# Kernel optimization log

Measured on AMD Instinct MI355X. Metric: run time of the kernel, lower is better.

The kernel has to match this reference:

```python
import jax, jax.numpy as jnp
import numpy as np

D_MODEL = 2048
N_HEADS = 16
N_KV_HEADS = 4
HEAD_DIM = D_MODEL // N_HEADS  # 128
ROPE_BASE = 10000.0


def _rope_tables(T, head_dim):
    half = head_dim // 2
    theta = 1.0 / (ROPE_BASE ** (jnp.arange(half, dtype=jnp.float32) / half))
    m = jnp.arange(T, dtype=jnp.float32)
    freqs = jnp.outer(m, theta)  # (T, half)
    return jnp.cos(freqs), jnp.sin(freqs)


def _apply_rope(x, cos, sin):
    # x: (B, H, T, hd); rotate first/second halves as pairs
    half = x.shape[-1] // 2
    x1, x2 = x[..., :half], x[..., half:]
    cos = cos[None, None, :, :]
    sin = sin[None, None, :, :]
    return jnp.concatenate([x1 * cos - x2 * sin, x1 * sin + x2 * cos], axis=-1)


def setup_inputs() -> dict:
    key = jax.random.key(0)
    ks = jax.random.split(key, 5)
    B, T = 4, 2048
    x = jax.random.normal(ks[0], (B, T, D_MODEL), dtype=jnp.float32)
    Wq = jax.random.normal(ks[1], (D_MODEL, N_HEADS * HEAD_DIM), dtype=jnp.float32) * 0.02
    Wk = jax.random.normal(ks[2], (D_MODEL, N_KV_HEADS * HEAD_DIM), dtype=jnp.float32) * 0.02
    Wv = jax.random.normal(ks[3], (D_MODEL, N_KV_HEADS * HEAD_DIM), dtype=jnp.float32) * 0.02
    Wo = jax.random.normal(ks[4], (N_HEADS * HEAD_DIM, D_MODEL), dtype=jnp.float32) * (0.02 / np.sqrt(2.0))
    return {"x": x, "Wq": Wq, "Wk": Wk, "Wv": Wv, "Wo": Wo}


def reference(x, Wq, Wk, Wv, Wo):
    B, T, C = x.shape
    groups = N_HEADS // N_KV_HEADS

    # QKV projections
    q = (x @ Wq).reshape(B, T, N_HEADS, HEAD_DIM).transpose(0, 2, 1, 3)      # (B,H,T,hd)
    k = (x @ Wk).reshape(B, T, N_KV_HEADS, HEAD_DIM).transpose(0, 2, 1, 3)   # (B,Hkv,T,hd)
    v = (x @ Wv).reshape(B, T, N_KV_HEADS, HEAD_DIM).transpose(0, 2, 1, 3)

    # RoPE on q and k
    cos, sin = _rope_tables(T, HEAD_DIM)
    q = _apply_rope(q, cos, sin)
    k = _apply_rope(k, cos, sin)

    # GQA: repeat each kv head `groups` times
    k = jnp.repeat(k, groups, axis=1)  # (B,H,T,hd)
    v = jnp.repeat(v, groups, axis=1)

    # Attention scores with ALiBi bias and causal mask
    scale = 1.0 / np.sqrt(HEAD_DIM)
    scores = jnp.einsum('bhqd,bhkd->bhqk', q, k) * scale  # (B,H,T,T)

    pos = jnp.arange(T)
    dist = jnp.minimum(pos[None, :] - pos[:, None], 0).astype(jnp.float32)  # (T,T), <=0
    slopes = 2.0 ** (-8.0 * jnp.arange(1, N_HEADS + 1, dtype=jnp.float32) / N_HEADS)
    alibi = slopes[:, None, None] * dist[None, :, :]  # (H,T,T)
    scores = scores + alibi[None]

    causal = pos[None, :] > pos[:, None]  # True = future = blocked
    scores = jnp.where(causal[None, None], -jnp.inf, scores)

    weights = jax.nn.softmax(scores, axis=-1)
    out = jnp.einsum('bhqk,bhkd->bhqd', weights, v)  # (B,H,T,hd)
    out = out.transpose(0, 2, 1, 3).reshape(B, T, N_HEADS * HEAD_DIM)
    return out @ Wo
```

## Files before the change

### kernel.cpp

```cpp
#include <hip/hip_runtime.h>
#include <hip/hip_bf16.h>
#include <stdint.h>

#define T_SEQ 2048
#define DM    2048
#define NH    16
#define NKVH  4
#define HD    128
#define NBATCH 4
#define BT    (NBATCH * T_SEQ)
#define ATT_SCALE 0.08838834764831845f
#define LOG2E 1.4426950408889634f

typedef __attribute__((ext_vector_type(8))) short bf16x8;
typedef __attribute__((ext_vector_type(4))) float f32x4;
typedef __attribute__((ext_vector_type(16))) float f32x16;
typedef __attribute__((ext_vector_type(8))) unsigned short ushort8;
typedef __attribute__((ext_vector_type(4))) unsigned short ushort4v;

static __device__ __forceinline__ unsigned short f2bf(float f) {
  __hip_bfloat16 h = __float2bfloat16(f);
  return __builtin_bit_cast(unsigned short, h);
}
static __device__ __forceinline__ float bf2f(unsigned short u) {
  unsigned int v = ((unsigned int)u) << 16;
  return __builtin_bit_cast(float, v);
}
static __device__ __forceinline__ unsigned int cvtpk(float a, float b) {
  unsigned int r;
  asm("v_cvt_pk_bf16_f32 %0, %1, %2" : "=v"(r) : "v"(a), "v"(b));
  return r;
}

#define GLDS16(g, l)                                                        \
  __builtin_amdgcn_global_load_lds(                                         \
      (const __attribute__((address_space(1))) void*)(g),                   \
      (__attribute__((address_space(3))) void*)(l), 16, 0, 0)

__global__ __launch_bounds__(256) void castx_k(const float* __restrict__ x,
                                               unsigned short* __restrict__ xb) {
  int i = (blockIdx.x * 256 + threadIdx.x) * 4;
  float4 v = *(const float4*)&x[i];
  ushort4v o;
  o[0] = f2bf(v.x); o[1] = f2bf(v.y); o[2] = f2bf(v.z); o[3] = f2bf(v.w);
  *(ushort4v*)&xb[i] = o;
}

__global__ __launch_bounds__(256) void transqkv_k(const float* __restrict__ Wq,
                                                  const float* __restrict__ Wk,
                                                  const float* __restrict__ Wv,
                                                  unsigned short* __restrict__ wqt) {
  __shared__ unsigned short t[64][72];
  const int bx = blockIdx.x;
  const float* src;
  unsigned short* dst;
  int ncols, n0;
  if (bx < 32) {
    src = Wq; dst = wqt; ncols = 2048; n0 = bx * 64;
  } else if (bx < 40) {
    src = Wk; dst = wqt + (size_t)2048 * 2048; ncols = 512; n0 = (bx - 32) * 64;
  } else {
    src = Wv; dst = wqt + (size_t)2560 * 2048; ncols = 512; n0 = (bx - 40) * 64;
  }
  const int r0 = blockIdx.y * 64;
  const int tid = threadIdx.x;
  const int tx = tid & 15, ty = tid >> 4;
#pragma unroll
  for (int i = 0; i < 4; i++) {
    int r = ty * 4 + i;
    float4 v = *(const float4*)&src[(size_t)(r0 + r) * ncols + n0 + tx * 4];
    t[r][tx * 4 + 0] = f2bf(v.x);
    t[r][tx * 4 + 1] = f2bf(v.y);
    t[r][tx * 4 + 2] = f2bf(v.z);
    t[r][tx * 4 + 3] = f2bf(v.w);
  }
  __syncthreads();
  int nl = tid >> 2, seg = tid & 3;
  ushort8 o0, o1;
#pragma unroll
  for (int j = 0; j < 8; j++) {
    o0[j] = t[seg * 16 + j][nl];
    o1[j] = t[seg * 16 + 8 + j][nl];
  }
  size_t base = (size_t)(n0 + nl) * 2048 + r0 + seg * 16;
  *(ushort8*)&dst[base] = o0;
  *(ushort8*)&dst[base + 8] = o1;
}

__global__ __launch_bounds__(256) void transw_k(const float* __restrict__ src,
                                                unsigned short* __restrict__ dst,
                                                int ncols) {
  __shared__ unsigned short t[64][72];
  int n0 = blockIdx.x * 64, r0 = blockIdx.y * 64;
  int tid = threadIdx.x;
  int tx = tid & 15, ty = tid >> 4;
#pragma unroll
  for (int i = 0; i < 4; i++) {
    int r = ty * 4 + i;
    float4 v = *(const float4*)&src[(size_t)(r0 + r) * ncols + n0 + tx * 4];
    t[r][tx * 4 + 0] = f2bf(v.x);
    t[r][tx * 4 + 1] = f2bf(v.y);
    t[r][tx * 4 + 2] = f2bf(v.z);
    t[r][tx * 4 + 3] = f2bf(v.w);
  }
  __syncthreads();
  int nl = tid >> 2, seg = tid & 3;
  ushort8 o0, o1;
#pragma unroll
  for (int j = 0; j < 8; j++) {
    o0[j] = t[seg * 16 + j][nl];
    o1[j] = t[seg * 16 + 8 + j][nl];
  }
  size_t base = (size_t)(n0 + nl) * 2048 + r0 + seg * 16;
  *(ushort8*)&dst[base] = o0;
  *(ushort8*)&dst[base + 8] = o1;
}

template <int EPI, int NBY, int BYG>
__global__ __launch_bounds__(512) void gemm8_k(const unsigned short* __restrict__ A,
                                               const unsigned short* __restrict__ Bt,
                                               unsigned short* __restrict__ q_out,
                                               unsigned short* __restrict__ k_out,
                                               unsigned short* __restrict__ v_out,
                                               float* __restrict__ f_out) {
  __shared__ __align__(16) unsigned short smem[65536];

  const int tid = threadIdx.x;
  const int lane = tid & 63, wid = tid >> 6;
  const int wm = wid >> 2, wn = wid & 3;
  const int lr = lane & 15, lq = lane >> 4;
  const int sw = ((lr >> 2) & 1) << 1;

  const int k8 = blockIdx.x & 7;
  const int l = blockIdx.x >> 3;
  const int gi = l / (4 * BYG);
  const int t4 = l % (4 * BYG);
  const int bx = k8 * 4 + (t4 & 3);
  const int by = gi * BYG + (t4 >> 2);
  const int row0 = bx * 256, n00 = by * 256;

  const int clog = (tid & 7) ^ (((tid >> 5) & 1) << 1);
  const unsigned short* Asrc = A + (size_t)row0 * 2048 + clog * 8;
  const unsigned short* Bsrc = Bt + (size_t)n00 * 2048 + clog * 8;

  auto stageA = [&](int buf, int h, int k0) {
#pragma unroll
    for (int c = 0; c < 2; c++) {
      const int rl = c * 128 + h * 64 + (tid >> 3);
      GLDS16(Asrc + (size_t)rl * 2048 + k0,
             &smem[buf * 32768 + (c * 128 + h * 64) * 64 + tid * 8]);
    }
  };
  auto stageB = [&](int buf, int h, int k0) {
#pragma unroll
    for (int c = 0; c < 2; c++) {
      const int pr = h * 128 + c * 64 + (tid >> 3);
      const int p = pr >> 5;
      const int lg = (p < 4) ? (2 * p) : (2 * (p - 4) + 1);
      const int logical = lg * 32 + (pr & 31);
      GLDS16(Bsrc + (size_t)logical * 2048 + k0,
             &smem[buf * 32768 + 16384 + (h * 128 + c * 64) * 64 + tid * 8]);
    }
  };

  auto ldA = [&](int buf, int rl, int kh) -> bf16x8 {
    return *(const bf16x8*)&smem[buf * 32768 + rl * 64 + (((kh << 2) + lq) ^ sw) * 8];
  };
  auto ldB = [&](int buf, int ni, int kh) -> bf16x8 {
    const int p = (ni < 2) ? wn : (4 + wn);
    const int pr = p * 32 + (ni & 1) * 16 + lr;
    return *(const bf16x8*)&smem[buf * 32768 + 16384 + pr * 64 +
                                 (((kh << 2) + lq) ^ sw) * 8];
  };

  f32x4 acc[8][4] = {};

  stageA(0, 0, 0);
  stageB(0, 0, 0);
  stageB(0, 1, 0);
  stageA(0, 1, 0);

  bf16x8 af[4][2], bfr[4][2];

#pragma unroll 1
  for (int t = 0; t < 32; ++t) {
    const int buf = t & 1, obuf = buf ^ 1;
    const bool nx = (t + 1 < 32);
    const int k0n = (t + 1) << 6;

    asm volatile("s_waitcnt vmcnt(4)" ::: "memory");
    asm volatile("s_barrier" ::: "memory");
#pragma unroll
    for (int m = 0; m < 4; m++)
#pragma unroll
      for (int kh = 0; kh < 2; kh++) af[m][kh] = ldA(buf, wm * 128 + m * 16 + lr, kh);
#pragma unroll
    for (int ni = 0; ni < 2; ni++)
#pragma unroll
      for (int kh = 0; kh < 2; kh++) bfr[ni][kh] = ldB(buf, ni, kh);
    if (nx) stageA(obuf, 0, k0n);
    __builtin_amdgcn_s_setprio(1);
#pragma unroll
    for (int m = 0; m < 4; m++)
#pragma unroll
      for (int ni = 0; ni < 2; ni++)
#pragma unroll
        for (int kh = 0; kh < 2; kh++)
          acc[m][ni] = __builtin_amdgcn_mfma_f32_16x16x32_bf16(af[m][kh], bfr[ni][kh],
                                                               acc[m][ni], 0, 0, 0);
    __builtin_amdgcn_s_setprio(0);

    if (nx) asm volatile("s_waitcnt vmcnt(4)" ::: "memory");
    else    asm volatile("s_waitcnt vmcnt(2)" ::: "memory");
    asm volatile("s_barrier" ::: "memory");
#pragma unroll
    for (int ni = 2; ni < 4; ni++)
#pragma unroll
      for (int kh = 0; kh < 2; kh++) bfr[ni][kh] = ldB(buf, ni, kh);
    if (nx) stageB(obuf, 0, k0n);
    __builtin_amdgcn_s_setprio(1);
#pragma unroll
    for (int m = 0; m < 4; m++)
#pragma unroll
      for (int ni = 2; ni < 4; ni++)
#pragma unroll
        for (int kh = 0; kh < 2; kh++)
          acc[m][ni] = __builtin_amdgcn_mfma_f32_16x16x32_bf16(af[m][kh], bfr[ni][kh],
                                                               acc[m][ni], 0, 0, 0);
    __builtin_amdgcn_s_setprio(0);

    if (nx) asm volatile("s_waitcnt vmcnt(4)" ::: "memory");
    else    asm volatile("s_waitcnt vmcnt(0)" ::: "memory");
    asm volatile("s_barrier" ::: "memory");
#pragma unroll
    for (int m = 0; m < 4; m++)
#pragma unroll
      for (int kh = 0; kh < 2; kh++)
        af[m][kh] = ldA(buf, wm * 128 + 64 + m * 16 + lr, kh);
    if (nx) stageB(obuf, 1, k0n);
    __builtin_amdgcn_s_setprio(1);
#pragma unroll
    for (int m = 0; m < 4; m++)
#pragma unroll
      for (int ni = 0; ni < 2; ni++)
#pragma unroll
        for (int kh = 0; kh < 2; kh++)
          acc[4 + m][ni] = __builtin_amdgcn_mfma_f32_16x16x32_bf16(
              af[m][kh], bfr[ni][kh], acc[4 + m][ni], 0, 0, 0);
    __builtin_amdgcn_s_setprio(0);

    asm volatile("s_barrier" ::: "memory");
    if (nx) stageA(obuf, 1, k0n);
    __builtin_amdgcn_s_setprio(1);
#pragma unroll
    for (int m = 0; m < 4; m++)
#pragma unroll
      for (int ni = 2; ni < 4; ni++)
#pragma unroll
        for (int kh = 0; kh < 2; kh++)
          acc[4 + m][ni] = __builtin_amdgcn_mfma_f32_16x16x32_bf16(
              af[m][kh], bfr[ni][kh], acc[4 + m][ni], 0, 0, 0);
    __builtin_amdgcn_s_setprio(0);
  }

  const int rbase = row0 + wm * 128;
  const int cbase = n00 + wn * 64;
#pragma unroll
  for (int mi = 0; mi < 8; mi++)
#pragma unroll
    for (int ni = 0; ni < 4; ni++)
#pragma unroll
      for (int r = 0; r < 4; r++) {
        int row = rbase + mi * 16 + lq * 4 + r;
        int col = cbase + ni * 16 + lr;
        float v = acc[mi][ni][r];
        if (EPI == 0) {
          if (col < 2048) {
            q_out[(size_t)row * 2048 + col] = f2bf(v);
          } else if (col < 2560) {
            k_out[(size_t)row * 512 + (col - 2048)] = f2bf(v);
          } else {
            int nv = col - 2560;
            int kvh = nv >> 7, d = nv & 127;
            int b = row >> 11, tt = row & 2047;
            v_out[((size_t)(b * NKVH + kvh) * HD + d) * T_SEQ + tt] = f2bf(v);
          }
        } else {
          f_out[(size_t)row * 2048 + col] = v;
        }
      }
}

__global__ __launch_bounds__(256) void rope_tab_k(float2* __restrict__ tab) {
  int idx = blockIdx.x * 256 + threadIdx.x;
  int t = idx >> 6, i = idx & 63;
  float theta = exp2f(-(float)i * (13.287712379549449f / 64.0f));
  float s, c;
  sincosf((float)t * theta, &s, &c);
  tab[idx] = make_float2(c, s);
}

__global__ __launch_bounds__(256) void ropek_k(unsigned short* __restrict__ kb,
                                               const float2* __restrict__ tab) {
  int idx = blockIdx.x * 256 + threadIdx.x;
  int i = idx & 63;
  int wi = idx >> 6;
  int kvh = wi & 3;
  int bt = wi >> 2;
  int t = bt & (T_SEQ - 1);
  unsigned short* p = kb + (size_t)bt * 512 + kvh * HD;
  float2 cs = tab[(t << 6) + i];
  float x1 = bf2f(p[i]), x2 = bf2f(p[i + 64]);
  p[i] = f2bf(x1 * cs.x - x2 * cs.y);
  p[i + 64] = f2bf(x1 * cs.y + x2 * cs.x);
}

__global__ __launch_bounds__(256) void attn_k(const unsigned short* __restrict__ qb,
                                              const unsigned short* __restrict__ kb,
                                              const unsigned short* __restrict__ vt,
                                              const float2* __restrict__ rtab,
                                              unsigned short* __restrict__ ao) {
  __shared__ __align__(16) unsigned short smem[24576];

  const int bid = blockIdx.x;
  const int j = 15 - (bid >> 6);
  const int g = (bid & 7) | (((bid >> 3) & 1) << 3);
  const int hh = (bid >> 4) & 3;
  const int b = g >> 2, kvh = g & 3;
  const int h = kvh * 4 + hh;

  const int tid = threadIdx.x;
  const int wid = tid >> 6, lane = tid & 63;
  const int l31 = lane & 31, lh = lane >> 5;
  const int xr = l31 & 7;
  const float slope2 = exp2f(-0.5f * (float)(h + 1)) * LOG2E;
  const float scale2 = ATT_SCALE * LOG2E;

  const int q0 = j * 128 + wid * 32;
  const int dt_w = j * 4 + wid;
  const int nt = j * 4 + 4;

  const int krow = tid >> 4;
  const int cgk = (tid & 15) ^ (krow & 7);
  const int vr = tid >> 3;
  const int cgv = (tid & 7) ^ (vr & 7);

  const unsigned short* khead = kb + (size_t)(b * T_SEQ) * 512 + kvh * 128;
  const unsigned short* vhead = vt + (size_t)(b * NKVH + kvh) * HD * T_SEQ;

  auto stage = [&](int slot, int tile) {
    const int k0 = tile * 32;
    unsigned short* base = &smem[slot * 8192];
    GLDS16(khead + (size_t)(k0 + krow) * 512 + cgk * 8, base + tid * 8);
    GLDS16(khead + (size_t)(k0 + 16 + krow) * 512 + cgk * 8, base + 2048 + tid * 8);
    GLDS16(vhead + (size_t)(((cgv >> 2) << 6) + vr) * T_SEQ + k0 + (cgv & 3) * 8,
           base + 4096 + tid * 8);
    GLDS16(vhead + (size_t)(((cgv >> 2) << 6) + 32 + vr) * T_SEQ + k0 + (cgv & 3) * 8,
           base + 6144 + tid * 8);
  };

  unsigned short (*ot)[32][136] = (unsigned short(*)[32][136])smem;

  stage(0, nt - 1);
  stage(1, nt - 2);

  const unsigned short* qrow =
      qb + ((size_t)(b * T_SEQ + q0 + l31)) * 2048 + h * HD + lh * 8;
  bf16x8 qf[8];
#pragma unroll
  for (int ds = 0; ds < 8; ds++) qf[ds] = *(const bf16x8*)&qrow[ds * 16];

  {
    const float2* rt = rtab + ((q0 + l31) << 6) + lh * 8;
#pragma unroll
    for (int ds = 0; ds < 4; ds++)
#pragma unroll
      for (int e = 0; e < 8; e++) {
        float2 cs = rt[ds * 16 + e];
        float x1 = bf2f((unsigned short)qf[ds][e]);
        float x2 = bf2f((unsigned short)qf[ds + 4][e]);
        qf[ds][e] = (short)f2bf(x1 * cs.x - x2 * cs.y);
        qf[ds + 4][e] = (short)f2bf(x1 * cs.y + x2 * cs.x);
      }
  }

  f32x16 oacc[4] = {};
  float m2 = -1e30f, l_half = 0.f;
  const float arow = -slope2 * (float)(q0 + l31);

  float cr[16];
#pragma unroll
  for (int r = 0; r < 16; r++) {
    const int crow = (r & 3) + 8 * (r >> 2) + 4 * lh;
    cr[r] = fmaf(slope2, (float)crow, arow);
  }

#pragma unroll 1
  for (int it = 0; it < nt; ++it) {
    const int tt = nt - 1 - it;
    if (it == nt - 1) {
      asm volatile("s_waitcnt vmcnt(0)" ::: "memory");
    } else {
      asm volatile("s_waitcnt vmcnt(4)" ::: "memory");
    }
    asm volatile("s_barrier" ::: "memory");
    if (tt >= 2) stage((it + 2) % 3, tt - 2);

    if (tt <= dt_w) {
      const int slot = it % 3;
      const unsigned short* Kb = &smem[slot * 8192];
      const unsigned short* Vb = &smem[slot * 8192 + 4096];
      const int k0 = tt * 32;

      bf16x8 kf[8];
#pragma unroll
      for (int ds = 0; ds < 8; ds++)
        kf[ds] = *(const bf16x8*)&Kb[l31 * 128 + ((2 * ds + lh) ^ xr) * 8];

      __builtin_amdgcn_s_setprio(1);
      f32x16 sca = 0.f, scb = 0.f;
#pragma unroll
      for (int ds = 0; ds < 4; ds++)
        sca = __builtin_amdgcn_mfma_f32_32x32x16_bf16(kf[ds], qf[ds], sca, 0, 0, 0);
#pragma unroll
      for (int ds = 4; ds < 8; ds++)
        scb = __builtin_amdgcn_mfma_f32_32x32x16_bf16(kf[ds], qf[ds], scb, 0, 0, 0);
      __builtin_amdgcn_s_setprio(0);

      bf16x8 vf[4][2];
#pragma unroll
      for (int dt = 0; dt < 4; dt++)
#pragma unroll
        for (int ks = 0; ks < 2; ks++)
          vf[dt][ks] = *(const bf16x8*)&Vb[((dt & 1) * 32 + l31) * 64 +
                                           (((dt >> 1) * 4 + 2 * ks + lh) ^ xr) * 8];

      float s1[16];
#pragma unroll
      for (int r = 0; r < 16; r++) s1[r] = fmaf(sca[r] + scb[r], scale2, cr[r]);
      if (tt == dt_w) {
#pragma unroll
        for (int r = 0; r < 16; r++) {
          const int crow = (r & 3) + 8 * (r >> 2) + 4 * lh;
          if (crow > l31) s1[r] = -1e30f;
        }
      }

      float z = fmaf(slope2, (float)k0, -m2);

      float t8[8], t4[4];
#pragma unroll
      for (int i = 0; i < 8; i++) t8[i] = fmaxf(s1[i], s1[i + 8]);
#pragma unroll
      for (int i = 0; i < 4; i++) t4[i] = fmaxf(t8[i], t8[i + 4]);
      float mx = fmaxf(fmaxf(t4[0], t4[1]), fmaxf(t4[2], t4[3]));

      float pr[16];
#pragma unroll
      for (int r = 0; r < 16; r++) pr[r] = exp2f(s1[r] + z);

      mx = fmaxf(mx, __shfl_xor(mx, 32));
      if (__any(mx + z > 8.f)) {
        const float mt = (mx + z) + m2;
        const float mnew = fmaxf(m2, mt);
        const float corr = exp2f(m2 - mnew);
        l_half *= corr;
#pragma unroll
        for (int dt = 0; dt < 4; dt++) oacc[dt] *= corr;
        m2 = mnew;
        z = fmaf(slope2, (float)k0, -m2);
#pragma unroll
        for (int r = 0; r < 16; r++) pr[r] = exp2f(s1[r] + z);
      }

      float a8[8], a4[4];
#pragma unroll
      for (int i = 0; i < 8; i++) a8[i] = pr[i] + pr[i + 8];
#pragma unroll
      for (int i = 0; i < 4; i++) a4[i] = a8[i] + a8[i + 4];
      l_half += (a4[0] + a4[1]) + (a4[2] + a4[3]);

      unsigned int w[8];
#pragma unroll
      for (int i = 0; i < 8; i++) w[i] = cvtpk(pr[2 * i], pr[2 * i + 1]);
      const unsigned int ta = __shfl_xor(lh ? w[0] : w[2], 32);
      const unsigned int tb = __shfl_xor(lh ? w[1] : w[3], 32);
      const unsigned int tc = __shfl_xor(lh ? w[4] : w[6], 32);
      const unsigned int td = __shfl_xor(lh ? w[5] : w[7], 32);
      union U4 { unsigned int u[4]; bf16x8 v; } f0, f1;
      f0.u[0] = lh ? ta : w[0];
      f0.u[1] = lh ? tb : w[1];
      f0.u[2] = lh ? w[2] : ta;
      f0.u[3] = lh ? w[3] : tb;
      f1.u[0] = lh ? tc : w[4];
      f1.u[1] = lh ? td : w[5];
      f1.u[2] = lh ? w[6] : tc;
      f1.u[3] = lh ? w[7] : td;

      __builtin_amdgcn_s_setprio(1);
#pragma unroll
      for (int dt = 0; dt < 4; dt++) {
        oacc[dt] =
            __builtin_amdgcn_mfma_f32_32x32x16_bf16(vf[dt][0], f0.v, oacc[dt], 0, 0, 0);
        oacc[dt] =
            __builtin_amdgcn_mfma_f32_32x32x16_bf16(vf[dt][1], f1.v, oacc[dt], 0, 0, 0);
      }
      __builtin_amdgcn_s_setprio(0);
    }
  }

  const float l_tot = l_half + __shfl_xor(l_half, 32);
  const float inv = 1.0f / l_tot;
  __syncthreads();
#pragma unroll
  for (int dt = 0; dt < 4; dt++)
#pragma unroll
    for (int rg = 0; rg < 4; rg++) {
      ushort4v o;
#pragma unroll
      for (int jj = 0; jj < 4; jj++) o[jj] = f2bf(oacc[dt][rg * 4 + jj] * inv);
      *(ushort4v*)&ot[wid][l31][dt * 32 + rg * 8 + lh * 4] = o;
    }
  __syncthreads();
  const int rrow = lane >> 4, chunk = lane & 15;
#pragma unroll
  for (int ps = 0; ps < 8; ps++) {
    const int row = ps * 4 + rrow;
    ushort8 v = *(const ushort8*)&ot[wid][row][chunk * 8];
    *(ushort8*)&ao[((size_t)(b * T_SEQ + q0 + row)) * 2048 + h * HD + chunk * 8] = v;
  }
}

extern "C" void kernel_launch(void* const* d_in, const int* in_sizes, int n_in,
                              void* d_out, int out_size, void* d_ws, size_t ws_size,
                              hipStream_t stream) {
  const float* x = (const float*)d_in[0];
  const float* Wq = (const float*)d_in[1];
  const float* Wk = (const float*)d_in[2];
  const float* Wv = (const float*)d_in[3];
  const float* Wo = (const float*)d_in[4];

  char* w = (char*)d_ws;
  unsigned short* xb = (unsigned short*)w;
  unsigned short* wqt = (unsigned short*)(w + 33554432);
  unsigned short* qb = (unsigned short*)(w + 33554432 + 12582912);
  unsigned short* kb = (unsigned short*)(w + 33554432 + 12582912 + 33554432);
  unsigned short* vtb = (unsigned short*)(w + 33554432 + 12582912 + 33554432 + 8388608);
  float2* rtab = (float2*)(w + 33554432 + 8388608);

  castx_k<<<16384, 256, 0, stream>>>(x, xb);
  transqkv_k<<<dim3(48, 32), 256, 0, stream>>>(Wq, Wk, Wv, wqt);
  gemm8_k<0, 12, 3><<<384, 512, 0, stream>>>(xb, wqt, qb, kb, vtb, nullptr);
  rope_tab_k<<<512, 256, 0, stream>>>(rtab);
  ropek_k<<<8192, 256, 0, stream>>>(kb, rtab);
  transw_k<<<dim3(32, 32), 256, 0, stream>>>(Wo, wqt, 2048);
  attn_k<<<1024, 256, 0, stream>>>(qb, kb, vtb, rtab, xb);
  gemm8_k<1, 8, 4><<<256, 512, 0, stream>>>(xb, wqt, nullptr, nullptr, nullptr,
                                            (float*)d_out);
}
```

Baseline: 442.2 us.

## Replace QKV projection GEMM with 256x128-tile kernel using split B staging

Adds a new QKV projection GEMM kernel that uses 256x128 output tiles with 8 waves arranged 4x2, double-buffered LDS, and B staging split into two halves interleaved with MFMA phases. It launches 768 blocks instead of the previous 384-block wide-tile kernel. The aim is better occupancy or load balance across CUs and overlap of global loads with compute. The trade-off is less reuse per tile (more A reloads) and a scattered per-element epilogue store for the V transpose.

```diff
diff --git a/kernel.cpp b/kernel.cpp
--- a/kernel.cpp
+++ b/kernel.cpp
@@ -114,6 +114,138 @@
   size_t base = (size_t)(n0 + nl) * 2048 + r0 + seg * 16;
   *(ushort8*)&dst[base] = o0;
   *(ushort8*)&dst[base + 8] = o1;
+}
+
+__global__ __launch_bounds__(512) void gemm0n_k(const unsigned short* __restrict__ A,
+                                                const unsigned short* __restrict__ Bt,
+                                                unsigned short* __restrict__ q_out,
+                                                unsigned short* __restrict__ k_out,
+                                                unsigned short* __restrict__ v_out) {
+  __shared__ __align__(16) unsigned short smem[49152];
+
+  const int tid = threadIdx.x;
+  const int lane = tid & 63, wid = tid >> 6;
+  const int wm = wid >> 1, wn = wid & 1;
+  const int lr = lane & 15, lq = lane >> 4;
+  const int sw = ((lr >> 2) & 1) << 1;
+
+  const int k8 = blockIdx.x & 7;
+  const int l = blockIdx.x >> 3;
+  const int bx = k8 * 4 + (l & 3);
+  const int by = l >> 2;
+  const int row0 = bx * 256, n00 = by * 128;
+
+  const int clog = (tid & 7) ^ (((tid >> 5) & 1) << 1);
+  const unsigned short* Asrc = A + (size_t)row0 * 2048 + clog * 8;
+  const unsigned short* Bsrc = Bt + (size_t)n00 * 2048 + clog * 8;
+
+  auto stageA = [&](int buf, int k0) {
+#pragma unroll
+    for (int c = 0; c < 4; c++)
+      GLDS16(Asrc + (size_t)(c * 64 + (tid >> 3)) * 2048 + k0,
+             &smem[buf * 24576 + c * 4096 + tid * 8]);
+  };
+  auto stageB = [&](int buf, int h, int k0) {
+    const int pg = h * 2 + (tid >> 8);
+    const int lg = ((pg & 1) << 1) | (pg >> 1);
+    const int lrow = lg * 32 + ((tid >> 3) & 31);
+    GLDS16(Bsrc + (size_t)lrow * 2048 + k0,
+           &smem[buf * 24576 + 16384 + h * 4096 + tid * 8]);
+  };
+
+  auto ldA = [&](int buf, int m, int kh) -> bf16x8 {
+    const int row = wm * 64 + m * 16 + lr;
+    return *(const bf16x8*)&smem[buf * 24576 + row * 64 + (((kh << 2) + lq) ^ sw) * 8];
+  };
+  auto ldB = [&](int buf, int ni, int kh) -> bf16x8 {
+    const int lg = wn * 2 + (ni >> 1);
+    const int pg = ((lg & 1) << 1) | (lg >> 1);
+    const int prow = pg * 32 + (ni & 1) * 16 + lr;
+    return *(const bf16x8*)&smem[buf * 24576 + 16384 + prow * 64 +
+                                 (((kh << 2) + lq) ^ sw) * 8];
+  };
+
+  f32x4 acc[4][4] = {};
+
+  stageA(0, 0);
+  stageB(0, 0, 0);
+  stageB(0, 1, 0);
+
+  bf16x8 af[4][2], bfr[4][2];
+
+#pragma unroll 1
+  for (int t = 0; t < 32; ++t) {
+    const int buf = t & 1, obuf = buf ^ 1;
+    const bool nx = (t + 1 < 32);
+    const int k0n = (t + 1) << 6;
+
+    asm volatile("s_waitcnt vmcnt(1)" ::: "memory");
+    asm volatile("s_barrier" ::: "memory");
+#pragma unroll
+    for (int m = 0; m < 4; m++)
+#pragma unroll
+      for (int kh = 0; kh < 2; kh++) af[m][kh] = ldA(buf, m, kh);
+#pragma unroll
+    for (int ni = 0; ni < 2; ni++)
+#pragma unroll
+      for (int kh = 0; kh < 2; kh++) bfr[ni][kh] = ldB(buf, ni, kh);
+    if (nx) stageA(obuf, k0n);
+    __builtin_amdgcn_s_setprio(1);
+#pragma unroll
+    for (int m = 0; m < 4; m++)
+#pragma unroll
+      for (int ni = 0; ni < 2; ni++)
+#pragma unroll
+        for (int kh = 0; kh < 2; kh++)
+          acc[m][ni] = __builtin_amdgcn_mfma_f32_16x16x32_bf16(af[m][kh], bfr[ni][kh],
+                                                               acc[m][ni], 0, 0, 0);
+    __builtin_amdgcn_s_setprio(0);
+
+    if (nx) asm volatile("s_waitcnt vmcnt(4)" ::: "memory");
+    else    asm volatile("s_waitcnt vmcnt(0)" ::: "memory");
+    asm volatile("s_barrier" ::: "memory");
+#pragma unroll
+    for (int ni = 2; ni < 4; ni++)
+#pragma unroll
+      for (int kh = 0; kh < 2; kh++) bfr[ni][kh] = ldB(buf, ni, kh);
+    if (nx) {
+      stageB(obuf, 0, k0n);
+      stageB(obuf, 1, k0n);
+    }
+    __builtin_amdgcn_s_setprio(1);
+#pragma unroll
+    for (int m = 0; m < 4; m++)
+#pragma unroll
+      for (int ni = 2; ni < 4; ni++)
+#pragma unroll
+        for (int kh = 0; kh < 2; kh++)
+          acc[m][ni] = __builtin_amdgcn_mfma_f32_16x16x32_bf16(af[m][kh], bfr[ni][kh],
+                                                               acc[m][ni], 0, 0, 0);
+    __builtin_amdgcn_s_setprio(0);
+  }
+
+  const int rbase = row0 + wm * 64;
+  const int cbase = n00 + wn * 64;
+#pragma unroll
+  for (int mi = 0; mi < 4; mi++)
+#pragma unroll
+    for (int ni = 0; ni < 4; ni++)
+#pragma unroll
+      for (int r = 0; r < 4; r++) {
+        int row = rbase + mi * 16 + lq * 4 + r;
+        int col = cbase + ni * 16 + lr;
+        float v = acc[mi][ni][r];
+        if (col < 2048) {
+          q_out[(size_t)row * 2048 + col] = f2bf(v);
+        } else if (col < 2560) {
+          k_out[(size_t)row * 512 + (col - 2048)] = f2bf(v);
+        } else {
+          int nv = col - 2560;
+          int kvh = nv >> 7, d = nv & 127;
+          int b = row >> 11, tt = row & 2047;
+          v_out[((size_t)(b * NKVH + kvh) * HD + d) * T_SEQ + tt] = f2bf(v);
+        }
+      }
 }
 
 template <int EPI, int NBY, int BYG>
@@ -550,7 +682,7 @@
 
   castx_k<<<16384, 256, 0, stream>>>(x, xb);
   transqkv_k<<<dim3(48, 32), 256, 0, stream>>>(Wq, Wk, Wv, wqt);
-  gemm8_k<0, 12, 3><<<384, 512, 0, stream>>>(xb, wqt, qb, kb, vtb, nullptr);
+  gemm0n_k<<<768, 512, 0, stream>>>(xb, wqt, qb, kb, vtb);
   rope_tab_k<<<512, 256, 0, stream>>>(rtab);
   ropek_k<<<8192, 256, 0, stream>>>(kb, rtab);
   transw_k<<<dim3(32, 32), 256, 0, stream>>>(Wo, wqt, 2048);
```

Measured after the change: 422.8 us. 1.05x faster.
